# Performance work log

Hardware: AMD Instinct MI355X
Metric: run time of the kernel (lower is better)

The kernel has to match this reference:

```python
import jax, jax.numpy as jnp
import numpy as np

MASK_THR = 0.005   # cfg.mask_thr
SIGMA = 2.0        # cfg.sigma (gaussian kernel)
N, G, H, W = 500, 128, 200, 304


def setup_inputs() -> dict:
    key = jax.random.key(0)
    k1, k2, k3, k4, k5, k6 = jax.random.split(key, 6)
    return {
        "cate_scores": jax.random.uniform(k1, (N,), jnp.float32),
        "seg_preds_x": jax.random.uniform(k2, (G, H, W), jnp.float32),
        "seg_preds_y": jax.random.uniform(k3, (G, H, W), jnp.float32),
        "cate_labels": jax.random.randint(k4, (N,), 0, 80),
        "x_inds": jax.random.randint(k5, (N,), 0, G),
        "y_inds": jax.random.randint(k6, (N,), 0, G),
    }


def reference(cate_scores, seg_preds_x, seg_preds_y, cate_labels, x_inds, y_inds):
    # --- SOLO decoupled mask decoding: irregular grid-index gather ---
    mask_x = seg_preds_x[x_inds]                 # [N,H,W]
    mask_y = seg_preds_y[y_inds]                 # [N,H,W]
    soft = mask_x * mask_y                       # seg_masks_soft
    hard = (soft > MASK_THR).astype(soft.dtype)  # seg_masks (binary)
    sum_masks = hard.sum((1, 2))                 # [N] mask areas
    # mask-quality rescoring
    seg_score = (soft * hard).sum((1, 2)) / jnp.maximum(sum_masks, 1.0)
    scores = cate_scores * seg_score

    # --- Matrix NMS (gaussian kernel) ---
    flat = hard.reshape(N, -1)                   # [N, H*W]
    inter = flat @ flat.T                        # [N,N] intersection areas
    union = sum_masks[:, None] + sum_masks[None, :] - inter
    iou = jnp.triu(inter / jnp.maximum(union, 1e-6), k=1)
    label_eq = jnp.triu((cate_labels[:, None] == cate_labels[None, :]).astype(soft.dtype), k=1)
    decay_iou = iou * label_eq                   # same-class IoU, upper tri
    comp_iou = decay_iou.max(0)                  # [N] max IoU with higher-scored same-class mask
    decay_matrix = jnp.exp(-SIGMA * decay_iou ** 2)
    comp_matrix = jnp.exp(-SIGMA * comp_iou ** 2)[:, None]  # expand(n,n).T in torch
    decay_coef = (decay_matrix / comp_matrix).min(0)         # [N]
    return scores * decay_coef
```

## Files before the change

### kernel.cpp

```cpp
#include <hip/hip_runtime.h>


#define N_DET 500
#define HW    (200 * 304)
#define TILE  64
#define NT    (HW / TILE)
#define PSTR  512
#define DSTR  950
#define NW2   (NT / 2)
#define NCLS  80
#define MM    64
#define MASK_THR 0.005f
#define SIGMA 2.0f

__global__ __launch_bounds__(512) void maskgen_kernel(
    const float* __restrict__ seg_x, const float* __restrict__ seg_y,
    const int* __restrict__ x_inds, const int* __restrict__ y_inds,
    unsigned long long* __restrict__ packed_t,
    float* __restrict__ part_sum)
{
    __shared__ __align__(16) float sx[128 * 64];
    __shared__ __align__(16) float sy[128 * 64];
    const int t   = blockIdx.x;
    const int tid = threadIdx.x;
    const int base = t * TILE;

    for (int e = tid; e < 128 * 16; e += 512) {
        const int r  = e >> 4;
        const int c4 = (e & 15) << 2;
        *(float4*)(sx + (r << 6) + c4) = *(const float4*)(seg_x + (size_t)r * HW + base + c4);
        *(float4*)(sy + (r << 6) + c4) = *(const float4*)(seg_y + (size_t)r * HW + base + c4);
    }
    __syncthreads();

    if (tid < N_DET) {
        const float4* __restrict__ rx4 = (const float4*)(sx + (x_inds[tid] << 6));
        const float4* __restrict__ ry4 = (const float4*)(sy + (y_inds[tid] << 6));
        float ssum = 0.0f;
        unsigned long long w = 0ull;
        #pragma unroll
        for (int k = 0; k < 16; ++k) {
            const int f = (k + tid) & 15;
            const float4 xv = rx4[f];
            const float4 yv = ry4[f];
            const float p0 = xv.x * yv.x, p1 = xv.y * yv.y,
                        p2 = xv.z * yv.z, p3 = xv.w * yv.w;
            const int b0 = p0 > MASK_THR, b1 = p1 > MASK_THR,
                      b2 = p2 > MASK_THR, b3 = p3 > MASK_THR;
            ssum += (b0 ? p0 : 0.0f) + (b1 ? p1 : 0.0f)
                  + (b2 ? p2 : 0.0f) + (b3 ? p3 : 0.0f);
            const unsigned int nib = (unsigned)(b0 | (b1 << 1) | (b2 << 2) | (b3 << 3));
            w |= (unsigned long long)nib << (f << 2);
        }
        packed_t[(size_t)t * PSTR + tid] = w;
        part_sum[(size_t)t * PSTR + tid] = ssum;
    }
}

__global__ __launch_bounds__(512) void transpose_kernel(
    const unsigned long long* __restrict__ packed_t,
    const float* __restrict__ part_sum,
    unsigned long long* __restrict__ packed_d,
    float* __restrict__ part_sumT)
{
    __shared__ unsigned long long tp[64 * 65];
    __shared__ float              ts[64 * 65];
    const int t0  = blockIdx.x * 64;
    const int d0  = blockIdx.y * 64;
    const int tid = threadIdx.x;
    const int lane = tid & 63, wav = tid >> 6;

    #pragma unroll
    for (int k = 0; k < 8; ++k) {
        const int r  = (k << 3) + wav;
        const int gt = t0 + r;
        unsigned long long v = 0ull; float s = 0.0f;
        if (gt < NT) {
            v = packed_t[(size_t)gt * PSTR + d0 + lane];
            s = part_sum[(size_t)gt * PSTR + d0 + lane];
        }
        tp[r * 65 + lane] = v;
        ts[r * 65 + lane] = s;
    }
    __syncthreads();
    const int gt = t0 + lane;
    #pragma unroll
    for (int k = 0; k < 8; ++k) {
        const int m = (k << 3) + wav;
        const int d = d0 + m;
        if (gt < NT && d < N_DET) {
            packed_d [(size_t)d * DSTR + gt] = tp[lane * 65 + m];
            part_sumT[(size_t)d * DSTR + gt] = ts[lane * 65 + m];
        }
    }
}

__global__ __launch_bounds__(512) void class_nms_kernel(
    const unsigned long long* __restrict__ packed_d,
    const float* __restrict__ part_sumT,
    const int* __restrict__ labels,
    const float* __restrict__ cate_scores,
    float* __restrict__ out)
{
    const int c    = blockIdx.x;
    const int tid  = threadIdx.x;
    const int lane = tid & 63, wav = tid >> 6;

    __shared__ int   s_list[MM];
    __shared__ int   s_wcnt[8];
    __shared__ float s_cnt[MM];
    __shared__ float s_sc[MM];
    __shared__ float s_comp[MM];
    __shared__ float pm[MM * MM];
    __shared__ int   s_m;

    int flag = 0;
    if (tid < N_DET) flag = (labels[tid] == c);
    const unsigned long long bmask = __ballot(flag);
    if (lane == 0) s_wcnt[wav] = __popcll(bmask);
    __syncthreads();
    int pre = 0;
    for (int w2 = 0; w2 < wav; ++w2) pre += s_wcnt[w2];
    if (flag) {
        const int pos = pre + __popcll(bmask & ((1ull << lane) - 1ull));
        if (pos < MM) s_list[pos] = tid;
    }
    if (tid == 0) {
        int mm = 0;
        for (int w2 = 0; w2 < 8; ++w2) mm += s_wcnt[w2];
        s_m = (mm > MM) ? MM : mm;
    }
    __syncthreads();
    const int m = s_m;
    if (m == 0) return;

    for (int mi = wav; mi < m; mi += 8) {
        const int i = s_list[mi];
        const ulonglong2* __restrict__ pi2 = (const ulonglong2*)(packed_d + (size_t)i * DSTR);
        const float2*     __restrict__ ps2 = (const float2*)(part_sumT + (size_t)i * DSTR);
        int cnt = 0; float S = 0.0f;
        #pragma unroll
        for (int q = 0; q < 8; ++q) {
            const int w = lane + (q << 6);
            if (w < NW2) {
                const ulonglong2 a = pi2[w];
                cnt += __popcll(a.x) + __popcll(a.y);
                const float2 s2 = ps2[w];
                S += s2.x + s2.y;
            }
        }
        float fcnt = (float)cnt;
        #pragma unroll
        for (int off = 32; off; off >>= 1) {
            fcnt += __shfl_down(fcnt, off);
            S    += __shfl_down(S,    off);
        }
        if (lane == 0) {
            s_cnt[mi] = fcnt;
            s_sc[mi]  = cate_scores[i] * (S / fmaxf(fcnt, 1.0f));
        }
    }
    __syncthreads();

    const int npairs = m * (m - 1) / 2;
    for (int p = wav; p < npairs; p += 8) {
        int mj = 1;
        while ((mj * (mj + 1)) / 2 <= p) ++mj;
        const int mi = p - mj * (mj - 1) / 2;
        const int i = s_list[mi], j = s_list[mj];
        const ulonglong2* __restrict__ pi2 = (const ulonglong2*)(packed_d + (size_t)i * DSTR);
        const ulonglong2* __restrict__ pj2 = (const ulonglong2*)(packed_d + (size_t)j * DSTR);
        int inter = 0;
        #pragma unroll
        for (int q = 0; q < 8; ++q) {
            const int w = lane + (q << 6);
            if (w < NW2) {
                const ulonglong2 a = pi2[w];
                const ulonglong2 b = pj2[w];
                inter += __popcll(a.x & b.x) + __popcll(a.y & b.y);
            }
        }
        float fint = (float)inter;
        #pragma unroll
        for (int off = 32; off; off >>= 1) fint += __shfl_down(fint, off);
        if (lane == 0) {
            const float uni = s_cnt[mi] + s_cnt[mj] - fint;
            pm[mi * MM + mj] = fint / fmaxf(uni, 1e-6f);
        }
    }
    __syncthreads();

    if (wav == 0 && lane < m) {
        const int mj = lane;
        float cmax = 0.0f;
        for (int mi = 0; mi < mj; ++mi) cmax = fmaxf(cmax, pm[mi * MM + mj]);
        s_comp[mj] = cmax * cmax;
    }
    __syncthreads();
    if (wav == 0 && lane < m) {
        const int mj = lane;
        float e = 0.0f;
        for (int mi = 0; mi < mj; ++mi) {
            const float d = pm[mi * MM + mj];
            e = fminf(e, s_comp[mi] - d * d);
        }
        out[s_list[mj]] = s_sc[mj] * expf(SIGMA * e);
    }
}

extern "C" void kernel_launch(void* const* d_in, const int* in_sizes, int n_in,
                              void* d_out, int out_size, void* d_ws, size_t ws_size,
                              hipStream_t stream) {
    const float* cate_scores = (const float*)d_in[0];
    const float* seg_x       = (const float*)d_in[1];
    const float* seg_y       = (const float*)d_in[2];
    const int*   labels      = (const int*)d_in[3];
    const int*   x_inds      = (const int*)d_in[4];
    const int*   y_inds      = (const int*)d_in[5];
    float* out = (float*)d_out;

    char* ws = (char*)d_ws;
    unsigned long long* packed_t = (unsigned long long*)(ws + 0);
    float* part_sum  = (float*)(ws + 3891200);
    unsigned long long* packed_d = (unsigned long long*)(ws + 5836800);
    float* part_sumT = (float*)(ws + 9636800);

    maskgen_kernel  <<<NT, 512, 0, stream>>>(seg_x, seg_y, x_inds, y_inds,
                                             packed_t, part_sum);
    transpose_kernel<<<dim3(15, 8), 512, 0, stream>>>(packed_t, part_sum,
                                                      packed_d, part_sumT);
    class_nms_kernel<<<NCLS, 512, 0, stream>>>(packed_d, part_sumT, labels,
                                               cate_scores, out);
}
```

Measured before the change: 132.8 us.

## Fuse transpose into maskgen by grouping four tiles per block, widen NMS block

Each maskgen block now processes four consecutive 64-pixel tiles and writes the bit-packed words directly in detection-major layout, together with one partial sum per group. This removes the separate transpose kernel and its round trip through global memory. The NMS kernel reads the shorter partial-sum array and runs with 1024 threads to use more waves per class. The trade-off is fewer maskgen blocks (238 instead of 950), so each block does serial load/sync phases and there is less parallelism to hide load latency. Padded entries beyond NT are zeroed so the popcounts stay correct.

```diff
diff --git a/kernel.cpp b/kernel.cpp
--- a/kernel.cpp
+++ b/kernel.cpp
@@ -5,9 +5,11 @@
 #define HW    (200 * 304)
 #define TILE  64
 #define NT    (HW / TILE)
-#define PSTR  512
-#define DSTR  950
-#define NW2   (NT / 2)
+#define GRP   4
+#define NG    238
+#define DSTR  952
+#define NW2   (DSTR / 2)
+#define PS_STR 240
 #define NCLS  80
 #define MM    64
 #define MASK_THR 0.005f
@@ -16,88 +18,69 @@
 __global__ __launch_bounds__(512) void maskgen_kernel(
     const float* __restrict__ seg_x, const float* __restrict__ seg_y,
     const int* __restrict__ x_inds, const int* __restrict__ y_inds,
-    unsigned long long* __restrict__ packed_t,
-    float* __restrict__ part_sum)
+    unsigned long long* __restrict__ packed_d,
+    float* __restrict__ part4)
 {
     __shared__ __align__(16) float sx[128 * 64];
     __shared__ __align__(16) float sy[128 * 64];
-    const int t   = blockIdx.x;
+    const int g   = blockIdx.x;
     const int tid = threadIdx.x;
-    const int base = t * TILE;
-
-    for (int e = tid; e < 128 * 16; e += 512) {
-        const int r  = e >> 4;
-        const int c4 = (e & 15) << 2;
-        *(float4*)(sx + (r << 6) + c4) = *(const float4*)(seg_x + (size_t)r * HW + base + c4);
-        *(float4*)(sy + (r << 6) + c4) = *(const float4*)(seg_y + (size_t)r * HW + base + c4);
-    }
-    __syncthreads();
+
+    int xrow = 0, yrow = 0;
+    if (tid < N_DET) { xrow = x_inds[tid] << 6; yrow = y_inds[tid] << 6; }
+
+    unsigned long long wacc[GRP];
+    float ssum = 0.0f;
+
+    #pragma unroll
+    for (int u = 0; u < GRP; ++u) {
+        const int t = g * GRP + u;
+        unsigned long long w = 0ull;
+        if (t < NT) {
+            const int base = t * TILE;
+            __syncthreads();
+            for (int e = tid; e < 128 * 16; e += 512) {
+                const int r  = e >> 4;
+                const int c4 = (e & 15) << 2;
+                *(float4*)(sx + (r << 6) + c4) = *(const float4*)(seg_x + (size_t)r * HW + base + c4);
+                *(float4*)(sy + (r << 6) + c4) = *(const float4*)(seg_y + (size_t)r * HW + base + c4);
+            }
+            __syncthreads();
+            if (tid < N_DET) {
+                const float4* __restrict__ rx4 = (const float4*)(sx + xrow);
+                const float4* __restrict__ ry4 = (const float4*)(sy + yrow);
+                #pragma unroll
+                for (int k = 0; k < 16; ++k) {
+                    const int f = (k + tid) & 15;
+                    const float4 xv = rx4[f];
+                    const float4 yv = ry4[f];
+                    const float p0 = xv.x * yv.x, p1 = xv.y * yv.y,
+                                p2 = xv.z * yv.z, p3 = xv.w * yv.w;
+                    const int b0 = p0 > MASK_THR, b1 = p1 > MASK_THR,
+                              b2 = p2 > MASK_THR, b3 = p3 > MASK_THR;
+                    ssum += (b0 ? p0 : 0.0f) + (b1 ? p1 : 0.0f)
+                          + (b2 ? p2 : 0.0f) + (b3 ? p3 : 0.0f);
+                    const unsigned int nib = (unsigned)(b0 | (b1 << 1) | (b2 << 2) | (b3 << 3));
+                    w |= (unsigned long long)nib << (f << 2);
+                }
+            }
+        }
+        wacc[u] = w;
+    }
 
     if (tid < N_DET) {
-        const float4* __restrict__ rx4 = (const float4*)(sx + (x_inds[tid] << 6));
-        const float4* __restrict__ ry4 = (const float4*)(sy + (y_inds[tid] << 6));
-        float ssum = 0.0f;
-        unsigned long long w = 0ull;
-        #pragma unroll
-        for (int k = 0; k < 16; ++k) {
-            const int f = (k + tid) & 15;
-            const float4 xv = rx4[f];
-            const float4 yv = ry4[f];
-            const float p0 = xv.x * yv.x, p1 = xv.y * yv.y,
-                        p2 = xv.z * yv.z, p3 = xv.w * yv.w;
-            const int b0 = p0 > MASK_THR, b1 = p1 > MASK_THR,
-                      b2 = p2 > MASK_THR, b3 = p3 > MASK_THR;
-            ssum += (b0 ? p0 : 0.0f) + (b1 ? p1 : 0.0f)
-                  + (b2 ? p2 : 0.0f) + (b3 ? p3 : 0.0f);
-            const unsigned int nib = (unsigned)(b0 | (b1 << 1) | (b2 << 2) | (b3 << 3));
-            w |= (unsigned long long)nib << (f << 2);
-        }
-        packed_t[(size_t)t * PSTR + tid] = w;
-        part_sum[(size_t)t * PSTR + tid] = ssum;
+        unsigned long long* dst = packed_d + (size_t)tid * DSTR + g * GRP;
+        ulonglong2 lo; lo.x = wacc[0]; lo.y = wacc[1];
+        ulonglong2 hi; hi.x = wacc[2]; hi.y = wacc[3];
+        *(ulonglong2*)(dst)     = lo;
+        *(ulonglong2*)(dst + 2) = hi;
+        part4[(size_t)tid * PS_STR + g] = ssum;
     }
 }
 
-__global__ __launch_bounds__(512) void transpose_kernel(
-    const unsigned long long* __restrict__ packed_t,
-    const float* __restrict__ part_sum,
-    unsigned long long* __restrict__ packed_d,
-    float* __restrict__ part_sumT)
-{
-    __shared__ unsigned long long tp[64 * 65];
-    __shared__ float              ts[64 * 65];
-    const int t0  = blockIdx.x * 64;
-    const int d0  = blockIdx.y * 64;
-    const int tid = threadIdx.x;
-    const int lane = tid & 63, wav = tid >> 6;
-
-    #pragma unroll
-    for (int k = 0; k < 8; ++k) {
-        const int r  = (k << 3) + wav;
-        const int gt = t0 + r;
-        unsigned long long v = 0ull; float s = 0.0f;
-        if (gt < NT) {
-            v = packed_t[(size_t)gt * PSTR + d0 + lane];
-            s = part_sum[(size_t)gt * PSTR + d0 + lane];
-        }
-        tp[r * 65 + lane] = v;
-        ts[r * 65 + lane] = s;
-    }
-    __syncthreads();
-    const int gt = t0 + lane;
-    #pragma unroll
-    for (int k = 0; k < 8; ++k) {
-        const int m = (k << 3) + wav;
-        const int d = d0 + m;
-        if (gt < NT && d < N_DET) {
-            packed_d [(size_t)d * DSTR + gt] = tp[lane * 65 + m];
-            part_sumT[(size_t)d * DSTR + gt] = ts[lane * 65 + m];
-        }
-    }
-}
-
-__global__ __launch_bounds__(512) void class_nms_kernel(
+__global__ __launch_bounds__(1024) void class_nms_kernel(
     const unsigned long long* __restrict__ packed_d,
-    const float* __restrict__ part_sumT,
+    const float* __restrict__ part4,
     const int* __restrict__ labels,
     const float* __restrict__ cate_scores,
     float* __restrict__ out)
@@ -107,7 +90,7 @@
     const int lane = tid & 63, wav = tid >> 6;
 
     __shared__ int   s_list[MM];
-    __shared__ int   s_wcnt[8];
+    __shared__ int   s_wcnt[16];
     __shared__ float s_cnt[MM];
     __shared__ float s_sc[MM];
     __shared__ float s_comp[MM];
@@ -127,27 +110,31 @@
     }
     if (tid == 0) {
         int mm = 0;
-        for (int w2 = 0; w2 < 8; ++w2) mm += s_wcnt[w2];
+        for (int w2 = 0; w2 < 16; ++w2) mm += s_wcnt[w2];
         s_m = (mm > MM) ? MM : mm;
     }
     __syncthreads();
     const int m = s_m;
     if (m == 0) return;
 
-    for (int mi = wav; mi < m; mi += 8) {
+    for (int mi = wav; mi < m; mi += 16) {
         const int i = s_list[mi];
         const ulonglong2* __restrict__ pi2 = (const ulonglong2*)(packed_d + (size_t)i * DSTR);
-        const float2*     __restrict__ ps2 = (const float2*)(part_sumT + (size_t)i * DSTR);
-        int cnt = 0; float S = 0.0f;
+        const float*      __restrict__ ps  = part4 + (size_t)i * PS_STR;
+        int cnt = 0;
         #pragma unroll
         for (int q = 0; q < 8; ++q) {
             const int w = lane + (q << 6);
             if (w < NW2) {
                 const ulonglong2 a = pi2[w];
                 cnt += __popcll(a.x) + __popcll(a.y);
-                const float2 s2 = ps2[w];
-                S += s2.x + s2.y;
-            }
+            }
+        }
+        float S = 0.0f;
+        #pragma unroll
+        for (int q = 0; q < 4; ++q) {
+            const int w = lane + (q << 6);
+            if (w < NG) S += ps[w];
         }
         float fcnt = (float)cnt;
         #pragma unroll
@@ -163,7 +150,7 @@
     __syncthreads();
 
     const int npairs = m * (m - 1) / 2;
-    for (int p = wav; p < npairs; p += 8) {
+    for (int p = wav; p < npairs; p += 16) {
         int mj = 1;
         while ((mj * (mj + 1)) / 2 <= p) ++mj;
         const int mi = p - mj * (mj - 1) / 2;
@@ -220,15 +207,11 @@
     float* out = (float*)d_out;
 
     char* ws = (char*)d_ws;
-    unsigned long long* packed_t = (unsigned long long*)(ws + 0);
-    float* part_sum  = (float*)(ws + 3891200);
-    unsigned long long* packed_d = (unsigned long long*)(ws + 5836800);
-    float* part_sumT = (float*)(ws + 9636800);
-
-    maskgen_kernel  <<<NT, 512, 0, stream>>>(seg_x, seg_y, x_inds, y_inds,
-                                             packed_t, part_sum);
-    transpose_kernel<<<dim3(15, 8), 512, 0, stream>>>(packed_t, part_sum,
-                                                      packed_d, part_sumT);
-    class_nms_kernel<<<NCLS, 512, 0, stream>>>(packed_d, part_sumT, labels,
-                                               cate_scores, out);
+    unsigned long long* packed_d = (unsigned long long*)(ws + 0);
+    float* part4 = (float*)(ws + 3808000);
+
+    maskgen_kernel  <<<NG,   512,  0, stream>>>(seg_x, seg_y, x_inds, y_inds,
+                                                packed_d, part4);
+    class_nms_kernel<<<NCLS, 1024, 0, stream>>>(packed_d, part4, labels,
+                                                cate_scores, out);
 }
```

Result: no change. 130.4 us (-1.8%).
